# Kernel optimization log

Measured on AMD Instinct MI355X. Metric: run time of the kernel, lower is better.

The kernel has to match this reference:

```python
import jax, jax.numpy as jnp
import numpy as np

B, C, N = 16, 512, 2048
C4 = C // 4
BN_EPS = 1e-5


def setup_inputs() -> dict:
    key = jax.random.key(0)
    ks = jax.random.split(key, 4)
    x = jax.random.normal(ks[0], (B, C, N), dtype=jnp.float32)
    # conv1d kernel_size=1 weights == dense matrices [out, in]
    wqk = jax.random.normal(ks[1], (C4, C), dtype=jnp.float32) * (1.0 / np.sqrt(C))
    wv = jax.random.normal(ks[2], (C, C), dtype=jnp.float32) * (1.0 / np.sqrt(C))
    bv = jnp.zeros((C,), dtype=jnp.float32)
    wt = jax.random.normal(ks[3], (C, C), dtype=jnp.float32) * (1.0 / np.sqrt(C))
    bt = jnp.zeros((C,), dtype=jnp.float32)
    gamma = jnp.ones((C,), dtype=jnp.float32)
    beta = jnp.zeros((C,), dtype=jnp.float32)
    return {"x": x, "wqk": wqk, "wv": wv, "bv": bv, "wt": wt, "bt": bt,
            "gamma": gamma, "beta": beta}


def reference(x, wqk, wv, bv, wt, bt, gamma, beta):
    # x: [B, C, N]
    # q_conv and k_conv share the same weight (aliased in the torch module)
    x_q = jnp.einsum('dc,bcn->bnd', wqk, x)          # [B, N, C4]
    x_k = jnp.einsum('dc,bcn->bdn', wqk, x)          # [B, C4, N]
    x_v = jnp.einsum('dc,bcn->bdn', wv, x) + bv[None, :, None]  # [B, C, N]

    energy = jnp.einsum('bnd,bdm->bnm', x_q, x_k)    # [B, N, N]
    attention = jax.nn.softmax(energy, axis=-1)
    # L1 renorm over the same (last) axis, as in the source
    attention = attention / (1e-9 + attention.sum(axis=2, keepdims=True))

    x_r = jnp.einsum('bcn,bnm->bcm', x_v, attention)  # x_v @ attention -> [B, C, N]

    t = jnp.einsum('dc,bcn->bdn', wt, x - x_r) + bt[None, :, None]  # trans_conv

    # BatchNorm1d in training mode: batch stats per channel over (B, N)
    mean = t.mean(axis=(0, 2), keepdims=True)
    var = t.var(axis=(0, 2), keepdims=True)
    t_hat = (t - mean) * jax.lax.rsqrt(var + BN_EPS)
    t_bn = t_hat * gamma[None, :, None] + beta[None, :, None]

    x_r = jax.nn.relu(t_bn)
    return x + x_r
```

## Files before the change

### kernel.cpp

```cpp
#include <hip/hip_runtime.h>


#define BB 16
#define CC 512
#define C4 128
#define NN 2048

typedef unsigned short u16;
typedef __attribute__((ext_vector_type(4))) unsigned short u16x4;
typedef __attribute__((ext_vector_type(8))) unsigned short u16x8;
typedef __attribute__((ext_vector_type(8))) short s16x8;
typedef __attribute__((ext_vector_type(4))) float f32x4;

#define MFMA(a, b, c) __builtin_amdgcn_mfma_f32_16x16x32_bf16((a), (b), (c), 0, 0, 0)

static __device__ __forceinline__ u16 f2bf(float f) {
    unsigned u = __float_as_uint(f);
    return (u16)((u + 0x7fffu + ((u >> 16) & 1u)) >> 16);
}
static __device__ __forceinline__ float bf2f(u16 h) {
    return __uint_as_float((unsigned)h << 16);
}
static __device__ __forceinline__ s16x8 ldfrag(const u16* __restrict__ p, size_t fi, int l) {
    return *reinterpret_cast<const s16x8*>(p + fi * 512 + l * 8);
}

static const size_t XKH_B  = 0;
static const size_t XKL_B  = 8388608;
static const size_t XVH_B  = 16777216;
static const size_t XVL_B  = 50331648;
static const size_t XT_B   = 83886080;
static const size_t W_B    = 150994944;
static const size_t RMAX_B = 153354240;
static const size_t RINV_B = RMAX_B + 131072;
static const size_t BNS_B  = RINV_B + 131072;
static const size_t BNQ_B  = BNS_B + 2048;
static const size_t SC_B   = BNQ_B + 2048;
static const size_t SH_B   = SC_B + 2048;

__global__ __launch_bounds__(256) void k_wsplit(
    const float* __restrict__ wqk, const float* __restrict__ wv,
    const float* __restrict__ wt, u16* __restrict__ wh, u16* __restrict__ wl)
{
    const int idx = blockIdx.x * 256 + threadIdx.x;
    const int e = idx * 4;
    const int row = e >> 9, col = e & 511;
    const float* src = (row < 128) ? (wqk + (size_t)row * 512 + col)
                     : (row < 640) ? (wv + (size_t)(row - 128) * 512 + col)
                                   : (wt + (size_t)(row - 640) * 512 + col);
    const float4 v = *(const float4*)src;
    u16x4 h, lo;
    h[0] = f2bf(v.x); lo[0] = f2bf(v.x - bf2f(h[0]));
    h[1] = f2bf(v.y); lo[1] = f2bf(v.y - bf2f(h[1]));
    h[2] = f2bf(v.z); lo[2] = f2bf(v.z - bf2f(h[2]));
    h[3] = f2bf(v.w); lo[3] = f2bf(v.w - bf2f(h[3]));
    const int g16 = row >> 4, rl = row & 15, kk = col >> 5, dcol = col & 31;
    const size_t off = ((size_t)g16 * 16 + kk) * 512 + ((dcol >> 3) * 16 + rl) * 8 + (dcol & 7);
    *(u16x4*)(wh + off) = h;
    *(u16x4*)(wl + off) = lo;
}

__global__ __launch_bounds__(256) void k_split_t(
    const float* __restrict__ src, u16* __restrict__ dsth, u16* __restrict__ dstl)
{
    __shared__ float S[64][69];
    const int b = blockIdx.z, rt = blockIdx.y, nt = blockIdx.x;
    const int tid = threadIdx.x;
    {
        const int rl = tid >> 2, c4 = (tid & 3) * 4;
        const float* sp = src + ((size_t)b * CC + rt * 64 + rl) * NN + nt * 64;
#pragma unroll
        for (int q = 0; q < 4; ++q) {
            const float4 v = *(const float4*)(sp + c4 + q * 16);
            const int col = c4 + q * 16;
            S[rl][col] = v.x; S[rl][col + 1] = v.y; S[rl][col + 2] = v.z; S[rl][col + 3] = v.w;
        }
    }
    __syncthreads();
    const int c0 = (tid & 7) * 8;
    const int cc = rt * 64 + c0;
    const int kk = cc >> 5, dcol = cc & 31;
#pragma unroll
    for (int p = 0; p < 2; ++p) {
        const int n_local = p * 32 + (tid >> 3);
        const int n = nt * 64 + n_local;
        u16x8 h, lo;
#pragma unroll
        for (int j = 0; j < 8; ++j) {
            const float v = S[c0 + j][n_local];
            const u16 hh = f2bf(v);
            h[j] = hh; lo[j] = f2bf(v - bf2f(hh));
        }
        const size_t off = (((size_t)b * 128 + (n >> 4)) * 16 + kk) * 512 +
                           ((dcol >> 3) * 16 + (n & 15)) * 8;
        *(u16x8*)(dsth + off) = h;
        *(u16x8*)(dstl + off) = lo;
    }
}

__global__ __launch_bounds__(256, 3) void k_proj_mfma(
    const u16* __restrict__ wh, const u16* __restrict__ wl,
    const u16* __restrict__ xth, const u16* __restrict__ xtl,
    const float* __restrict__ bv,
    u16* __restrict__ xkh, u16* __restrict__ xkl,
    u16* __restrict__ xvh, u16* __restrict__ xvl)
{
    __shared__ u16 Tt[128][136];
    const int b = blockIdx.z, mb = blockIdx.y, nb = blockIdx.x;
    const int tid = threadIdx.x;
    const int w = tid >> 6, l = tid & 63;
    const int l15 = l & 15, lg = l >> 4;
    const int wm = w >> 1, wn = w & 1;
    const int m0 = mb * 128 + wm * 64;
    const int n0 = nb * 128 + wn * 64;
    const u16* Bh = xth + (size_t)b * NN * CC;
    const u16* Bl = xtl + (size_t)b * NN * CC;

    f32x4 acc[4][4];
#pragma unroll
    for (int am = 0; am < 4; ++am)
#pragma unroll
        for (int an = 0; an < 4; ++an) acc[am][an] = (f32x4){0.f, 0.f, 0.f, 0.f};

    for (int kk = 0; kk < 16; ++kk) {
        s16x8 ah[4], al[4], bh4[4], bl4[4];
#pragma unroll
        for (int am = 0; am < 4; ++am) {
            const size_t fi = (size_t)(m0 / 16 + am) * 16 + kk;
            ah[am] = ldfrag(wh, fi, l);
            al[am] = ldfrag(wl, fi, l);
        }
#pragma unroll
        for (int an = 0; an < 4; ++an) {
            const size_t fi = (size_t)(n0 / 16 + an) * 16 + kk;
            bh4[an] = ldfrag(Bh, fi, l);
            bl4[an] = ldfrag(Bl, fi, l);
        }
#pragma unroll
        for (int am = 0; am < 4; ++am)
#pragma unroll
            for (int an = 0; an < 4; ++an) {
                acc[am][an] = MFMA(ah[am], bh4[an], acc[am][an]);
                acc[am][an] = MFMA(al[am], bh4[an], acc[am][an]);
                acc[am][an] = MFMA(ah[am], bl4[an], acc[am][an]);
            }
    }

    if (mb == 0) {
#pragma unroll
        for (int pass = 0; pass < 2; ++pass) {
            if (pass) __syncthreads();
#pragma unroll
            for (int am = 0; am < 4; ++am)
#pragma unroll
                for (int an = 0; an < 4; ++an) {
                    const int nl = wn * 64 + an * 16 + l15;
                    const int dbase = wm * 64 + am * 16 + lg * 4;
#pragma unroll
                    for (int r = 0; r < 4; ++r) {
                        const float v = acc[am][an][r];
                        const u16 h = f2bf(v);
                        Tt[nl][dbase + r] = pass ? f2bf(v - bf2f(h)) : h;
                    }
                }
            __syncthreads();
            u16* dst = pass ? xkl : xkh;
#pragma unroll
            for (int i = 0; i < 8; ++i) {
                const int flat = i * 256 + tid;
                const int g16l = flat >> 8;
                const int kk2  = (flat >> 6) & 3;
                const int ll   = flat & 63;
                const int row  = g16l * 16 + (ll & 15);
                const int col  = kk2 * 32 + (ll >> 4) * 8;
                const size_t fi = ((size_t)b * 128 + nb * 8 + g16l) * 4 + kk2;
                *(u16x8*)(dst + fi * 512 + ll * 8) = *(const u16x8*)&Tt[row][col];
            }
        }
    } else {
#pragma unroll
        for (int am = 0; am < 4; ++am) {
            const int cb = m0 - C4 + am * 16 + lg * 4;
#pragma unroll
            for (int r = 0; r < 4; ++r) {
                const int c = cb + r;
                const float bias = bv[c];
                const int cg = c >> 4, cl = c & 15;
#pragma unroll
                for (int an = 0; an < 4; ++an) {
                    const int n = n0 + an * 16 + l15;
                    const float v = acc[am][an][r] + bias;
                    const u16 h = f2bf(v);
                    const size_t off = (((size_t)b * 64 + (n >> 5)) * 32 + cg) * 512 +
                                       (((n & 31) >> 3) * 16 + cl) * 8 + (n & 7);
                    xvh[off] = h;
                    xvl[off] = f2bf(v - bf2f(h));
                }
            }
        }
    }
}

__global__ __launch_bounds__(256) void k_stats(
    const u16* __restrict__ xkh, const u16* __restrict__ xkl,
    float* __restrict__ rmax, float* __restrict__ rinv)
{
    const int b = blockIdx.y, nb = blockIdx.x;
    const int tid = threadIdx.x;
    const int w = tid >> 6, l = tid & 63;
    const int l15 = l & 15, lg = l >> 4;
    const u16* Hb = xkh + (size_t)b * NN * C4;
    const u16* Lb = xkl + (size_t)b * NN * C4;
    s16x8 ah[4], al[4];
#pragma unroll
    for (int kk = 0; kk < 4; ++kk) {
        const size_t fi = (size_t)(nb * 4 + w) * 4 + kk;
        ah[kk] = ldfrag(Hb, fi, l);
        al[kk] = ldfrag(Lb, fi, l);
    }
    float m[4], s[4];
#pragma unroll
    for (int r = 0; r < 4; ++r) { m[r] = -3.0e38f; s[r] = 0.0f; }

    for (int mt = 0; mt < NN / 64; ++mt) {
        f32x4 e[4];
#pragma unroll
        for (int ms = 0; ms < 4; ++ms) e[ms] = (f32x4){0.f, 0.f, 0.f, 0.f};
#pragma unroll
        for (int kk = 0; kk < 4; ++kk) {
#pragma unroll
            for (int ms = 0; ms < 4; ++ms) {
                const size_t fi = (size_t)(mt * 4 + ms) * 4 + kk;
                const s16x8 bh = ldfrag(Hb, fi, l);
                const s16x8 bl = ldfrag(Lb, fi, l);
                e[ms] = MFMA(ah[kk], bh, e[ms]);
                e[ms] = MFMA(al[kk], bh, e[ms]);
                e[ms] = MFMA(ah[kk], bl, e[ms]);
            }
        }
#pragma unroll
        for (int r = 0; r < 4; ++r) {
            const float v0 = e[0][r], v1 = e[1][r], v2 = e[2][r], v3 = e[3][r];
            const float vm = fmaxf(fmaxf(v0, v1), fmaxf(v2, v3));
            const float nm = fmaxf(m[r], vm);
            s[r] = s[r] * __expf(m[r] - nm) +
                   __expf(v0 - nm) + __expf(v1 - nm) + __expf(v2 - nm) + __expf(v3 - nm);
            m[r] = nm;
        }
    }
#pragma unroll
    for (int off = 1; off < 16; off <<= 1) {
#pragma unroll
        for (int r = 0; r < 4; ++r) {
            const float mo = __shfl_xor(m[r], off);
            const float so = __shfl_xor(s[r], off);
            const float nm = fmaxf(m[r], mo);
            s[r] = s[r] * __expf(m[r] - nm) + so * __expf(mo - nm);
            m[r] = nm;
        }
    }
    if (l15 == 0) {
        const size_t base = (size_t)b * NN + nb * 64 + w * 16 + lg * 4;
#pragma unroll
        for (int r = 0; r < 4; ++r) {
            rmax[base + r] = m[r];
            rinv[base + r] = 1.0f / (s[r] * (1.0f + 1e-9f));
        }
    }
}

__global__ __launch_bounds__(512, 2) void k_attn_pv(
    const u16* __restrict__ xkh, const u16* __restrict__ xkl,
    const u16* __restrict__ xvh, const u16* __restrict__ xvl,
    const float* __restrict__ x, const float* __restrict__ rmax,
    const float* __restrict__ rinv, float* __restrict__ u)
{
    __shared__ u16 pT[64][72];
    const int b = blockIdx.y, mb = blockIdx.x;
    const int tid = threadIdx.x;
    const int w = tid >> 6, l = tid & 63;
    const int l15 = l & 15, lg = l >> 4;
    const int nsub = w >> 1, jb = (w & 1) * 2;
    const int M0 = mb * 64;
    const u16* Hb = xkh + (size_t)b * NN * C4;
    const u16* Lb = xkl + (size_t)b * NN * C4;
    const u16* Vh = xvh + (size_t)b * CC * NN;
    const u16* Vl = xvl + (size_t)b * CC * NN;

    s16x8 bh[2][4], bl[2][4];
#pragma unroll
    for (int j = 0; j < 2; ++j) {
#pragma unroll
        for (int kk = 0; kk < 4; ++kk) {
            const size_t fi = (size_t)(mb * 4 + jb + j) * 4 + kk;
            bh[j][kk] = ldfrag(Hb, fi, l);
            bl[j][kk] = ldfrag(Lb, fi, l);
        }
    }
    f32x4 acc[4][4];
#pragma unroll
    for (int cs = 0; cs < 4; ++cs)
#pragma unroll
        for (int ms = 0; ms < 4; ++ms) acc[cs][ms] = (f32x4){0.f, 0.f, 0.f, 0.f};

    for (int nt = 0; nt < NN / 64; ++nt) {
        const int n0 = nt * 64;
        f32x4 e0 = {0.f, 0.f, 0.f, 0.f}, e1 = {0.f, 0.f, 0.f, 0.f};
#pragma unroll
        for (int kk = 0; kk < 4; ++kk) {
            const size_t fi = (size_t)(nt * 4 + nsub) * 4 + kk;
            const s16x8 ah = ldfrag(Hb, fi, l);
            const s16x8 al = ldfrag(Lb, fi, l);
            e0 = MFMA(ah, bh[0][kk], e0); e0 = MFMA(al, bh[0][kk], e0); e0 = MFMA(ah, bl[0][kk], e0);
            e1 = MFMA(ah, bh[1][kk], e1); e1 = MFMA(al, bh[1][kk], e1); e1 = MFMA(ah, bl[1][kk], e1);
        }
        const size_t rbase = (size_t)b * NN + n0 + nsub * 16 + lg * 4;
        const float4 rm = *(const float4*)(rmax + rbase);
        const float4 ri = *(const float4*)(rinv + rbase);
        u16x4 p0, p1;
        p0[0] = f2bf(__expf(e0[0] - rm.x) * ri.x);
        p0[1] = f2bf(__expf(e0[1] - rm.y) * ri.y);
        p0[2] = f2bf(__expf(e0[2] - rm.z) * ri.z);
        p0[3] = f2bf(__expf(e0[3] - rm.w) * ri.w);
        p1[0] = f2bf(__expf(e1[0] - rm.x) * ri.x);
        p1[1] = f2bf(__expf(e1[1] - rm.y) * ri.y);
        p1[2] = f2bf(__expf(e1[2] - rm.z) * ri.z);
        p1[3] = f2bf(__expf(e1[3] - rm.w) * ri.w);
        __syncthreads();
        const int ncol = nsub * 16 + lg * 4;
        *reinterpret_cast<u16x4*>(&pT[(jb + 0) * 16 + l15][ncol]) = p0;
        *reinterpret_cast<u16x4*>(&pT[(jb + 1) * 16 + l15][ncol]) = p1;
        __syncthreads();
#pragma unroll
        for (int kk = 0; kk < 2; ++kk) {
            const int nn = kk * 32 + lg * 8;
            s16x8 avh[4], avl[4];
#pragma unroll
            for (int cs = 0; cs < 4; ++cs) {
                const size_t fi = (size_t)(nt * 2 + kk) * 32 + (w * 4 + cs);
                avh[cs] = ldfrag(Vh, fi, l);
                avl[cs] = ldfrag(Vl, fi, l);
            }
#pragma unroll
            for (int ms = 0; ms < 4; ++ms) {
                const s16x8 bp = *reinterpret_cast<const s16x8*>(&pT[ms * 16 + l15][nn]);
#pragma unroll
                for (int cs = 0; cs < 4; ++cs) {
                    acc[cs][ms] = MFMA(avh[cs], bp, acc[cs][ms]);
                    acc[cs][ms] = MFMA(avl[cs], bp, acc[cs][ms]);
                }
            }
        }
    }
    const float* xb = x + (size_t)b * CC * NN;
    float* ub = u + (size_t)b * CC * NN;
#pragma unroll
    for (int cs = 0; cs < 4; ++cs) {
#pragma unroll
        for (int r = 0; r < 4; ++r) {
            const int c = w * 64 + cs * 16 + lg * 4 + r;
#pragma unroll
            for (int ms = 0; ms < 4; ++ms) {
                const size_t o = (size_t)c * NN + M0 + ms * 16 + l15;
                ub[o] = xb[o] - acc[cs][ms][r];
            }
        }
    }
}

__global__ __launch_bounds__(256, 3) void k_trans_mfma(
    const u16* __restrict__ wh, const u16* __restrict__ wl,
    const u16* __restrict__ uth, const u16* __restrict__ utl,
    const float* __restrict__ bt, float* __restrict__ t,
    float* __restrict__ bns, float* __restrict__ bnq)
{
    const int b = blockIdx.z, mb = blockIdx.y, nb = blockIdx.x;
    const int tid = threadIdx.x;
    const int w = tid >> 6, l = tid & 63;
    const int l15 = l & 15, lg = l >> 4;
    const int wm = w >> 1, wn = w & 1;
    const int m0 = mb * 128 + wm * 64;
    const int n0 = nb * 128 + wn * 64;
    const u16* Bh = uth + (size_t)b * NN * CC;
    const u16* Bl = utl + (size_t)b * NN * CC;

    f32x4 acc[4][4];
#pragma unroll
    for (int am = 0; am < 4; ++am)
#pragma unroll
        for (int an = 0; an < 4; ++an) acc[am][an] = (f32x4){0.f, 0.f, 0.f, 0.f};

    for (int kk = 0; kk < 16; ++kk) {
        s16x8 ah[4], al[4], bh4[4], bl4[4];
#pragma unroll
        for (int am = 0; am < 4; ++am) {
            const size_t fi = (size_t)(40 + m0 / 16 + am) * 16 + kk;
            ah[am] = ldfrag(wh, fi, l);
            al[am] = ldfrag(wl, fi, l);
        }
#pragma unroll
        for (int an = 0; an < 4; ++an) {
            const size_t fi = (size_t)(n0 / 16 + an) * 16 + kk;
            bh4[an] = ldfrag(Bh, fi, l);
            bl4[an] = ldfrag(Bl, fi, l);
        }
#pragma unroll
        for (int am = 0; am < 4; ++am)
#pragma unroll
            for (int an = 0; an < 4; ++an) {
                acc[am][an] = MFMA(ah[am], bh4[an], acc[am][an]);
                acc[am][an] = MFMA(al[am], bh4[an], acc[am][an]);
                acc[am][an] = MFMA(ah[am], bl4[an], acc[am][an]);
            }
    }

    float* tb = t + (size_t)b * CC * NN;
#pragma unroll
    for (int am = 0; am < 4; ++am) {
        const int cb = m0 + am * 16 + lg * 4;
        float rs[4], rq[4];
#pragma unroll
        for (int r = 0; r < 4; ++r) { rs[r] = 0.f; rq[r] = 0.f; }
#pragma unroll
        for (int r = 0; r < 4; ++r) {
            const int c = cb + r;
            const float bias = bt[c];
#pragma unroll
            for (int an = 0; an < 4; ++an) {
                const float v = acc[am][an][r] + bias;
                tb[(size_t)c * NN + n0 + an * 16 + l15] = v;
                rs[r] += v;
                rq[r] += v * v;
            }
        }
#pragma unroll
        for (int off = 1; off < 16; off <<= 1) {
#pragma unroll
            for (int r = 0; r < 4; ++r) {
                rs[r] += __shfl_xor(rs[r], off);
                rq[r] += __shfl_xor(rq[r], off);
            }
        }
        if (l15 == 0) {
#pragma unroll
            for (int r = 0; r < 4; ++r) {
                atomicAdd(&bns[cb + r], rs[r]);
                atomicAdd(&bnq[cb + r], rq[r]);
            }
        }
    }
}

__global__ void k_bnfin(const float* __restrict__ bns, const float* __restrict__ bnq,
                        const float* __restrict__ gamma, const float* __restrict__ beta,
                        float* __restrict__ scale, float* __restrict__ shift)
{
    const int c = threadIdx.x;
    if (c < CC) {
        const float inv = 1.0f / (float)(BB * NN);
        const float mean = bns[c] * inv;
        const float var = bnq[c] * inv - mean * mean;
        const float sc = gamma[c] * rsqrtf(var + 1e-5f);
        scale[c] = sc;
        shift[c] = beta[c] - mean * sc;
    }
}

__global__ __launch_bounds__(256) void k_out(
    const float* __restrict__ x, const float* __restrict__ t,
    const float* __restrict__ scale, const float* __restrict__ shift,
    float* __restrict__ out)
{
    const size_t total4 = (size_t)BB * CC * NN / 4;
    for (size_t idx = (size_t)blockIdx.x * blockDim.x + threadIdx.x; idx < total4;
         idx += (size_t)gridDim.x * blockDim.x) {
        const size_t e = idx * 4;
        const int c = (int)((e / NN) % CC);
        const float sc = scale[c], sh = shift[c];
        const float4 xq = ((const float4*)x)[idx];
        const float4 tq = ((const float4*)t)[idx];
        float4 o;
        o.x = xq.x + fmaxf(tq.x * sc + sh, 0.0f);
        o.y = xq.y + fmaxf(tq.y * sc + sh, 0.0f);
        o.z = xq.z + fmaxf(tq.z * sc + sh, 0.0f);
        o.w = xq.w + fmaxf(tq.w * sc + sh, 0.0f);
        ((float4*)out)[idx] = o;
    }
}

extern "C" void kernel_launch(void* const* d_in, const int* in_sizes, int n_in,
                              void* d_out, int out_size, void* d_ws, size_t ws_size,
                              hipStream_t stream)
{
    const float* x     = (const float*)d_in[0];
    const float* wqk   = (const float*)d_in[1];
    const float* wv    = (const float*)d_in[2];
    const float* bv    = (const float*)d_in[3];
    const float* wt    = (const float*)d_in[4];
    const float* bt    = (const float*)d_in[5];
    const float* gamma = (const float*)d_in[6];
    const float* beta  = (const float*)d_in[7];
    char* ws = (char*)d_ws;

    u16*   xkh  = (u16*)(ws + XKH_B);
    u16*   xkl  = (u16*)(ws + XKL_B);
    u16*   xvh  = (u16*)(ws + XVH_B);
    u16*   xvl  = (u16*)(ws + XVL_B);
    u16*   uth  = (u16*)(ws + XVH_B);
    u16*   utl  = (u16*)(ws + XVL_B);
    u16*   xth  = (u16*)(ws + XT_B);
    u16*   xtl  = (u16*)(ws + XT_B + 33554432);
    float* ub   = (float*)(ws + XT_B);
    float* t    = (float*)(ws + XT_B);
    u16*   wh   = (u16*)(ws + W_B);
    u16*   wl   = (u16*)(ws + W_B + 1179648);
    float* rmax = (float*)(ws + RMAX_B);
    float* rinv = (float*)(ws + RINV_B);
    float* bns  = (float*)(ws + BNS_B);
    float* bnq  = (float*)(ws + BNQ_B);
    float* sc   = (float*)(ws + SC_B);
    float* sh   = (float*)(ws + SH_B);

    hipMemsetAsync(bns, 0, 2 * CC * sizeof(float), stream);

    k_wsplit<<<576, 256, 0, stream>>>(wqk, wv, wt, wh, wl);
    k_split_t<<<dim3(32, 8, BB), 256, 0, stream>>>(x, xth, xtl);
    k_proj_mfma<<<dim3(16, 5, BB), 256, 0, stream>>>(wh, wl, xth, xtl, bv,
                                                     xkh, xkl, xvh, xvl);
    k_stats<<<dim3(32, BB), 256, 0, stream>>>(xkh, xkl, rmax, rinv);
    k_attn_pv<<<dim3(32, BB), 512, 0, stream>>>(xkh, xkl, xvh, xvl, x, rmax, rinv, ub);
    k_split_t<<<dim3(32, 8, BB), 256, 0, stream>>>(ub, uth, utl);
    k_trans_mfma<<<dim3(16, 4, BB), 256, 0, stream>>>(wh, wl, uth, utl, bt, t, bns, bnq);
    k_bnfin<<<1, 512, 0, stream>>>(bns, bnq, gamma, beta, sc, sh);
    k_out<<<2048, 256, 0, stream>>>(x, t, sc, sh, (float*)d_out);
}
```

Before: 729.6 us.

## Double-buffer attention probabilities and fuse hi/lo split into attention epilogue

The attention-PV kernel now double-buffers the shared-memory probability tile: it computes the next tile's energies and softmax while running the PV MFMAs on the current tile, which cuts the barriers per iteration from two to one. The epilogue writes the residual x - x_r straight into the bf16 hi/lo fragment layout, so the separate k_split_t pass and the fp32 intermediate round trip go away. Workspace buffers are reassigned to fit this. The cost is more registers and LDS per block, which could lower occupancy at 512 threads, and the epilogue scatters 2-byte stores.

```diff
diff --git a/kernel.cpp b/kernel.cpp
--- a/kernel.cpp
+++ b/kernel.cpp
@@ -273,9 +273,10 @@
     const u16* __restrict__ xkh, const u16* __restrict__ xkl,
     const u16* __restrict__ xvh, const u16* __restrict__ xvl,
     const float* __restrict__ x, const float* __restrict__ rmax,
-    const float* __restrict__ rinv, float* __restrict__ u)
-{
-    __shared__ u16 pT[64][72];
+    const float* __restrict__ rinv,
+    u16* __restrict__ uth, u16* __restrict__ utl)
+{
+    __shared__ u16 pT[2][64][72];
     const int b = blockIdx.y, mb = blockIdx.x;
     const int tid = threadIdx.x;
     const int w = tid >> 6, l = tid & 63;
@@ -297,40 +298,57 @@
             bl[j][kk] = ldfrag(Lb, fi, l);
         }
     }
-    f32x4 acc[4][4];
-#pragma unroll
-    for (int cs = 0; cs < 4; ++cs)
-#pragma unroll
-        for (int ms = 0; ms < 4; ++ms) acc[cs][ms] = (f32x4){0.f, 0.f, 0.f, 0.f};
-
-    for (int nt = 0; nt < NN / 64; ++nt) {
-        const int n0 = nt * 64;
-        f32x4 e0 = {0.f, 0.f, 0.f, 0.f}, e1 = {0.f, 0.f, 0.f, 0.f};
+
+    auto computeE = [&](int nt, f32x4& E0, f32x4& E1) {
+        E0 = (f32x4){0.f, 0.f, 0.f, 0.f};
+        E1 = (f32x4){0.f, 0.f, 0.f, 0.f};
 #pragma unroll
         for (int kk = 0; kk < 4; ++kk) {
             const size_t fi = (size_t)(nt * 4 + nsub) * 4 + kk;
             const s16x8 ah = ldfrag(Hb, fi, l);
             const s16x8 al = ldfrag(Lb, fi, l);
-            e0 = MFMA(ah, bh[0][kk], e0); e0 = MFMA(al, bh[0][kk], e0); e0 = MFMA(ah, bl[0][kk], e0);
-            e1 = MFMA(ah, bh[1][kk], e1); e1 = MFMA(al, bh[1][kk], e1); e1 = MFMA(ah, bl[1][kk], e1);
-        }
-        const size_t rbase = (size_t)b * NN + n0 + nsub * 16 + lg * 4;
+            E0 = MFMA(ah, bh[0][kk], E0); E0 = MFMA(al, bh[0][kk], E0); E0 = MFMA(ah, bl[0][kk], E0);
+            E1 = MFMA(ah, bh[1][kk], E1); E1 = MFMA(al, bh[1][kk], E1); E1 = MFMA(ah, bl[1][kk], E1);
+        }
+    };
+    auto softmaxWrite = [&](int nt, f32x4 E0, f32x4 E1) {
+        const size_t rbase = (size_t)b * NN + nt * 64 + nsub * 16 + lg * 4;
         const float4 rm = *(const float4*)(rmax + rbase);
         const float4 ri = *(const float4*)(rinv + rbase);
         u16x4 p0, p1;
-        p0[0] = f2bf(__expf(e0[0] - rm.x) * ri.x);
-        p0[1] = f2bf(__expf(e0[1] - rm.y) * ri.y);
-        p0[2] = f2bf(__expf(e0[2] - rm.z) * ri.z);
-        p0[3] = f2bf(__expf(e0[3] - rm.w) * ri.w);
-        p1[0] = f2bf(__expf(e1[0] - rm.x) * ri.x);
-        p1[1] = f2bf(__expf(e1[1] - rm.y) * ri.y);
-        p1[2] = f2bf(__expf(e1[2] - rm.z) * ri.z);
-        p1[3] = f2bf(__expf(e1[3] - rm.w) * ri.w);
-        __syncthreads();
+        p0[0] = f2bf(__expf(E0[0] - rm.x) * ri.x);
+        p0[1] = f2bf(__expf(E0[1] - rm.y) * ri.y);
+        p0[2] = f2bf(__expf(E0[2] - rm.z) * ri.z);
+        p0[3] = f2bf(__expf(E0[3] - rm.w) * ri.w);
+        p1[0] = f2bf(__expf(E1[0] - rm.x) * ri.x);
+        p1[1] = f2bf(__expf(E1[1] - rm.y) * ri.y);
+        p1[2] = f2bf(__expf(E1[2] - rm.z) * ri.z);
+        p1[3] = f2bf(__expf(E1[3] - rm.w) * ri.w);
+        const int buf = nt & 1;
         const int ncol = nsub * 16 + lg * 4;
-        *reinterpret_cast<u16x4*>(&pT[(jb + 0) * 16 + l15][ncol]) = p0;
-        *reinterpret_cast<u16x4*>(&pT[(jb + 1) * 16 + l15][ncol]) = p1;
-        __syncthreads();
+        *reinterpret_cast<u16x4*>(&pT[buf][(jb + 0) * 16 + l15][ncol]) = p0;
+        *reinterpret_cast<u16x4*>(&pT[buf][(jb + 1) * 16 + l15][ncol]) = p1;
+    };
+
+    f32x4 acc[4][4];
+#pragma unroll
+    for (int cs = 0; cs < 4; ++cs)
+#pragma unroll
+        for (int ms = 0; ms < 4; ++ms) acc[cs][ms] = (f32x4){0.f, 0.f, 0.f, 0.f};
+
+    {
+        f32x4 e0, e1;
+        computeE(0, e0, e1);
+        softmaxWrite(0, e0, e1);
+    }
+    __syncthreads();
+
+    for (int nt = 0; nt < NN / 64; ++nt) {
+        const int n0 = nt * 64;
+        const int buf = nt & 1;
+        const bool more = (nt + 1) < NN / 64;
+        f32x4 ne0, ne1;
+        if (more) computeE(nt + 1, ne0, ne1);
 #pragma unroll
         for (int kk = 0; kk < 2; ++kk) {
             const int nn = kk * 32 + lg * 8;
@@ -343,7 +361,7 @@
             }
 #pragma unroll
             for (int ms = 0; ms < 4; ++ms) {
-                const s16x8 bp = *reinterpret_cast<const s16x8*>(&pT[ms * 16 + l15][nn]);
+                const s16x8 bp = *reinterpret_cast<const s16x8*>(&pT[buf][ms * 16 + l15][nn]);
 #pragma unroll
                 for (int cs = 0; cs < 4; ++cs) {
                     acc[cs][ms] = MFMA(avh[cs], bp, acc[cs][ms]);
@@ -351,9 +369,11 @@
                 }
             }
         }
-    }
+        if (more) softmaxWrite(nt + 1, ne0, ne1);
+        __syncthreads();
+    }
+
     const float* xb = x + (size_t)b * CC * NN;
-    float* ub = u + (size_t)b * CC * NN;
 #pragma unroll
     for (int cs = 0; cs < 4; ++cs) {
 #pragma unroll
@@ -361,8 +381,13 @@
             const int c = w * 64 + cs * 16 + lg * 4 + r;
 #pragma unroll
             for (int ms = 0; ms < 4; ++ms) {
-                const size_t o = (size_t)c * NN + M0 + ms * 16 + l15;
-                ub[o] = xb[o] - acc[cs][ms][r];
+                const int n = M0 + ms * 16 + l15;
+                const float v = xb[(size_t)c * NN + n] - acc[cs][ms][r];
+                const u16 h = f2bf(v);
+                const size_t off = (((size_t)b * 128 + (n >> 4)) * 16 + (c >> 5)) * 512 +
+                                   (((c & 31) >> 3) * 16 + (n & 15)) * 8 + (c & 7);
+                uth[off] = h;
+                utl[off] = f2bf(v - bf2f(h));
             }
         }
     }
@@ -506,12 +531,11 @@
     u16*   xkl  = (u16*)(ws + XKL_B);
     u16*   xvh  = (u16*)(ws + XVH_B);
     u16*   xvl  = (u16*)(ws + XVL_B);
-    u16*   uth  = (u16*)(ws + XVH_B);
-    u16*   utl  = (u16*)(ws + XVL_B);
     u16*   xth  = (u16*)(ws + XT_B);
     u16*   xtl  = (u16*)(ws + XT_B + 33554432);
-    float* ub   = (float*)(ws + XT_B);
-    float* t    = (float*)(ws + XT_B);
+    u16*   uth  = (u16*)(ws + XT_B);
+    u16*   utl  = (u16*)(ws + XT_B + 33554432);
+    float* t    = (float*)(ws + XVH_B);
     u16*   wh   = (u16*)(ws + W_B);
     u16*   wl   = (u16*)(ws + W_B + 1179648);
     float* rmax = (float*)(ws + RMAX_B);
@@ -528,8 +552,8 @@
     k_proj_mfma<<<dim3(16, 5, BB), 256, 0, stream>>>(wh, wl, xth, xtl, bv,
                                                      xkh, xkl, xvh, xvl);
     k_stats<<<dim3(32, BB), 256, 0, stream>>>(xkh, xkl, rmax, rinv);
-    k_attn_pv<<<dim3(32, BB), 512, 0, stream>>>(xkh, xkl, xvh, xvl, x, rmax, rinv, ub);
-    k_split_t<<<dim3(32, 8, BB), 256, 0, stream>>>(ub, uth, utl);
+    k_attn_pv<<<dim3(32, BB), 512, 0, stream>>>(xkh, xkl, xvh, xvl, x, rmax, rinv,
+                                                uth, utl);
     k_trans_mfma<<<dim3(16, 4, BB), 256, 0, stream>>>(wh, wl, uth, utl, bt, t, bns, bnq);
     k_bnfin<<<1, 512, 0, stream>>>(bns, bnq, gamma, beta, sc, sh);
     k_out<<<2048, 256, 0, stream>>>(x, t, sc, sh, (float*)d_out);
```

Result: faster. 708.2 us (-2.9%).
